# Kernel tuning notes

Hardware: AMD Instinct MI355X
Metric: run time of the kernel (lower is better)

Reference implementation:

```python
import jax, jax.numpy as jnp
import numpy as np

D = H = W = 40          # spatial grid (D,H,W)
KP = 2048               # static capacity for pred indices (pred > EPS)
KT = 40960              # static capacity for true indices (true > 0)
EPS = 2.0               # threshold (init kwarg epsilon)
BIG = 1e30              # sentinel distance^2 for invalid true slots


def setup_inputs() -> dict:
    key = jax.random.key(0)
    k1, k2 = jax.random.split(key)
    inp = jax.random.normal(k1, (2, D, H, W), dtype=jnp.float32)
    tgt = jax.random.normal(k2, (2, D, H, W), dtype=jnp.float32)
    return {"input": inp, "target": tgt}


def _coords(flat_idx):
    # flat voxel index -> (z, y, x) float coordinates; clamp fill (-1) to 0 (masked later)
    i = jnp.maximum(flat_idx, 0)
    z = i // (H * W)
    y = (i // W) % H
    x = i % W
    return jnp.stack([z, y, x], axis=-1).astype(jnp.float32)  # [K, 3]


def _per_batch(pred_flat, true_flat):
    # thresholded nonzero index sets (static-size, padded with -1)
    p_idx = jnp.nonzero(pred_flat > EPS, size=KP, fill_value=-1)[0]
    t_idx = jnp.nonzero(true_flat > 0.0, size=KT, fill_value=-1)[0]
    p_valid = p_idx >= 0
    t_valid = t_idx >= 0
    P = _coords(p_idx)  # [KP, 3]
    T = _coords(t_idx)  # [KT, 3]
    # squared euclidean distances via ||a||^2 + ||b||^2 - 2 a.b  (matmul form of cdist)
    d2 = ((P * P).sum(-1)[:, None]
          + (T * T).sum(-1)[None, :]
          - 2.0 * (P @ T.T))                    # [KP, KT]
    d2 = jnp.where(t_valid[None, :], jnp.maximum(d2, 0.0), BIG)
    min_d = jnp.sqrt(jnp.min(d2, axis=1))       # 1-NN distance per pred point
    n_true = t_valid.sum()
    # original: if no true points, distances are all zero
    min_d = jnp.where(n_true > 0, min_d, 0.0)
    s = jnp.where(p_valid, min_d, 0.0).sum()
    return s, p_valid.sum()


def reference(input, target):
    B = input.shape[0]
    pf = input.reshape(B, -1)
    tf = target.reshape(B, -1)
    sums, counts = jax.vmap(_per_batch)(pf, tf)
    total = sums.sum()
    cnt = counts.sum()
    # mean over all concatenated distances; 0.0 if no pred point passes threshold
    return jnp.where(cnt > 0, total / jnp.maximum(cnt, 1).astype(jnp.float32), 0.0)
```

## Files before the change

kernel.cpp:

```cpp
#include <hip/hip_runtime.h>
#include <math.h>

#define DDIM  40
#define HWsz  1600
#define NVOX  64000
#define NB    2
#define EPSV  2.0f
#define NWORD 1000
#define NBLK  (NB * NVOX / 256)
#define INF_I 0x7fffffff

struct Ws {
  unsigned long long tmask[NB * NWORD];
  float sum;
  int   cnt;
  int   done;
};

__global__ void mask_k(const float* __restrict__ tgt, Ws* __restrict__ ws) {
  int gid = blockIdx.x * blockDim.x + threadIdx.x;
  if (gid == 0) { ws->sum = 0.0f; ws->cnt = 0; ws->done = 0; }
  unsigned long long m = __ballot(tgt[gid] > 0.0f);
  if ((threadIdx.x & 63) == 0) ws->tmask[gid >> 6] = m;
}

__global__ void nn_k(const float* __restrict__ inp, Ws* __restrict__ ws,
                     float* __restrict__ out) {
  int gid = blockIdx.x * blockDim.x + threadIdx.x;
  int b = gid / NVOX;
  int v = gid - b * NVOX;
  bool pred = inp[gid] > EPSV;

  float dist = 0.0f;
  if (pred) {
    int pz = v / HWsz;
    int r  = v - pz * HWsz;
    int py = r / DDIM;
    int px = r - py * DDIM;
    const unsigned long long* __restrict__ tm = ws->tmask + b * NWORD;
    int best = INF_I;
    for (int s = 0; s < DDIM; ++s) {
      if (s * s > best) break;
      for (int dz = -s; dz <= s; ++dz) {
        int zz = pz + dz;
        if ((unsigned)zz >= (unsigned)DDIM) continue;
        int edgez = (dz == -s) | (dz == s);
        for (int dy = -s; dy <= s; ++dy) {
          int yy = py + dy;
          if ((unsigned)yy >= (unsigned)DDIM) continue;
          int stepx = (edgez | (dy == -s) | (dy == s)) ? 1 : 2 * s;
          for (int dx = -s; dx <= s; dx += stepx) {
            int xx = px + dx;
            if ((unsigned)xx >= (unsigned)DDIM) continue;
            int vv = zz * HWsz + yy * DDIM + xx;
            if ((tm[vv >> 6] >> (vv & 63)) & 1ull) {
              int d2 = dz * dz + dy * dy + dx * dx;
              best = min(best, d2);
            }
          }
        }
      }
    }
    if (best != INF_I) dist = sqrtf((float)best);
  }

  for (int o = 32; o > 0; o >>= 1) dist += __shfl_down(dist, o, 64);
  int wcount = __popcll(__ballot(pred));

  __shared__ float lsum[4];
  __shared__ int   lcnt[4];
  int lane = threadIdx.x & 63, wid = threadIdx.x >> 6;
  if (lane == 0) { lsum[wid] = dist; lcnt[wid] = wcount; }
  __syncthreads();
  if (threadIdx.x == 0) {
    float bs = lsum[0] + lsum[1] + lsum[2] + lsum[3];
    int   bc = lcnt[0] + lcnt[1] + lcnt[2] + lcnt[3];
    if (bs != 0.0f) atomicAdd(&ws->sum, bs);
    if (bc != 0)    atomicAdd(&ws->cnt, bc);
    __threadfence();
    int prev = atomicAdd(&ws->done, 1);
    if (prev == NBLK - 1) {
      float s = atomicAdd(&ws->sum, 0.0f);
      int   c = atomicAdd(&ws->cnt, 0);
      out[0] = (c > 0) ? s / (float)c : 0.0f;
    }
  }
}

extern "C" void kernel_launch(void* const* d_in, const int* in_sizes, int n_in,
                              void* d_out, int out_size, void* d_ws, size_t ws_size,
                              hipStream_t stream) {
  const float* inp = (const float*)d_in[0];
  const float* tgt = (const float*)d_in[1];
  float* out = (float*)d_out;
  Ws* ws = (Ws*)d_ws;

  hipLaunchKernelGGL(mask_k, dim3(NBLK), dim3(256), 0, stream, tgt, ws);
  hipLaunchKernelGGL(nn_k,   dim3(NBLK), dim3(256), 0, stream, inp, ws, out);
}
```

Baseline: 79.40 us.

## Drop target bitmask pass and search target floats directly with unrolled first shell

Removes the separate kernel that packed the target into a bitmask and replaces it with a one-thread init kernel. The search kernel now reads target floats directly: it returns early when the voxel itself is a target, checks the 26 neighbours in a fully unrolled shell, and falls back to the expanding-shell search only when none of them is a target. This cuts a full pass over the target and a dependent load chain, at the cost of reading 4-byte floats instead of packed bits. Radius-1 hits are very likely with this random data, so the fallback should rarely run.

```diff
diff --git a/kernel.cpp b/kernel.cpp
--- a/kernel.cpp
+++ b/kernel.cpp
@@ -6,56 +6,71 @@
 #define NVOX  64000
 #define NB    2
 #define EPSV  2.0f
-#define NWORD 1000
 #define NBLK  (NB * NVOX / 256)
 #define INF_I 0x7fffffff
 
 struct Ws {
-  unsigned long long tmask[NB * NWORD];
   float sum;
   int   cnt;
   int   done;
 };
 
-__global__ void mask_k(const float* __restrict__ tgt, Ws* __restrict__ ws) {
-  int gid = blockIdx.x * blockDim.x + threadIdx.x;
-  if (gid == 0) { ws->sum = 0.0f; ws->cnt = 0; ws->done = 0; }
-  unsigned long long m = __ballot(tgt[gid] > 0.0f);
-  if ((threadIdx.x & 63) == 0) ws->tmask[gid >> 6] = m;
+__global__ void init_k(Ws* ws) {
+  if (threadIdx.x == 0) { ws->sum = 0.0f; ws->cnt = 0; ws->done = 0; }
 }
 
-__global__ void nn_k(const float* __restrict__ inp, Ws* __restrict__ ws,
-                     float* __restrict__ out) {
+__global__ void nn_k(const float* __restrict__ inp,
+                     const float* __restrict__ tgt,
+                     Ws* __restrict__ ws, float* __restrict__ out) {
   int gid = blockIdx.x * blockDim.x + threadIdx.x;
   int b = gid / NVOX;
   int v = gid - b * NVOX;
   bool pred = inp[gid] > EPSV;
 
   float dist = 0.0f;
-  if (pred) {
+  if (pred && !(tgt[gid] > 0.0f)) {
     int pz = v / HWsz;
     int r  = v - pz * HWsz;
     int py = r / DDIM;
     int px = r - py * DDIM;
-    const unsigned long long* __restrict__ tm = ws->tmask + b * NWORD;
+    const float* __restrict__ tb = tgt + b * NVOX;
     int best = INF_I;
-    for (int s = 0; s < DDIM; ++s) {
-      if (s * s > best) break;
-      for (int dz = -s; dz <= s; ++dz) {
-        int zz = pz + dz;
-        if ((unsigned)zz >= (unsigned)DDIM) continue;
-        int edgez = (dz == -s) | (dz == s);
-        for (int dy = -s; dy <= s; ++dy) {
-          int yy = py + dy;
-          if ((unsigned)yy >= (unsigned)DDIM) continue;
-          int stepx = (edgez | (dy == -s) | (dy == s)) ? 1 : 2 * s;
-          for (int dx = -s; dx <= s; dx += stepx) {
-            int xx = px + dx;
-            if ((unsigned)xx >= (unsigned)DDIM) continue;
-            int vv = zz * HWsz + yy * DDIM + xx;
-            if ((tm[vv >> 6] >> (vv & 63)) & 1ull) {
-              int d2 = dz * dz + dy * dy + dx * dx;
-              best = min(best, d2);
+
+    #pragma unroll
+    for (int dz = -1; dz <= 1; ++dz)
+      #pragma unroll
+      for (int dy = -1; dy <= 1; ++dy)
+        #pragma unroll
+        for (int dx = -1; dx <= 1; ++dx) {
+          if (dz == 0 && dy == 0 && dx == 0) continue;
+          int zz = pz + dz, yy = py + dy, xx = px + dx;
+          bool ok = (unsigned)zz < (unsigned)DDIM &&
+                    (unsigned)yy < (unsigned)DDIM &&
+                    (unsigned)xx < (unsigned)DDIM;
+          if (ok && tb[zz * HWsz + yy * DDIM + xx] > 0.0f) {
+            int d2 = dz * dz + dy * dy + dx * dx;
+            best = min(best, d2);
+          }
+        }
+
+    if (best == INF_I) {
+      for (int s = 2; s < DDIM; ++s) {
+        if ((long long)s * s > (long long)best) break;
+        for (int dz = -s; dz <= s; ++dz) {
+          int zz = pz + dz;
+          if ((unsigned)zz >= (unsigned)DDIM) continue;
+          int edgez = (dz == -s) | (dz == s);
+          for (int dy = -s; dy <= s; ++dy) {
+            int yy = py + dy;
+            if ((unsigned)yy >= (unsigned)DDIM) continue;
+            int stepx = (edgez | (dy == -s) | (dy == s)) ? 1 : 2 * s;
+            for (int dx = -s; dx <= s; dx += stepx) {
+              int xx = px + dx;
+              if ((unsigned)xx >= (unsigned)DDIM) continue;
+              if (tb[zz * HWsz + yy * DDIM + xx] > 0.0f) {
+                int d2 = dz * dz + dy * dy + dx * dx;
+                best = min(best, d2);
+              }
             }
           }
         }
@@ -95,6 +110,6 @@
   float* out = (float*)d_out;
   Ws* ws = (Ws*)d_ws;
 
-  hipLaunchKernelGGL(mask_k, dim3(NBLK), dim3(256), 0, stream, tgt, ws);
-  hipLaunchKernelGGL(nn_k,   dim3(NBLK), dim3(256), 0, stream, inp, ws, out);
+  hipLaunchKernelGGL(init_k, dim3(1), dim3(64), 0, stream, ws);
+  hipLaunchKernelGGL(nn_k,   dim3(NBLK), dim3(256), 0, stream, inp, tgt, ws, out);
 }
```

New measurement: 78.55 us. Within noise of the previous version (-1.1%).
